# Performance work log

Measured on AMD Instinct MI355X. Metric: run time of the kernel, lower is better.

Reference implementation:

```python
import jax, jax.numpy as jnp
import numpy as np

B, S, H, K = 64, 512, 1024, 7

def setup_inputs() -> dict:
    key = jax.random.key(0)
    ks = jax.random.split(key, 7)
    x = jax.random.normal(ks[0], (B, S, H), dtype=jnp.float32)
    gt = jax.random.randint(ks[1], (B, S), 0, K, dtype=jnp.int64)
    mask = jnp.ones((B, S), dtype=bool)
    # learned parameters
    W = jax.random.normal(ks[2], (H, K), dtype=jnp.float32) * (1.0 / np.sqrt(H))
    b = jnp.zeros((K,), dtype=jnp.float32)
    start_trans = jax.random.uniform(ks[3], (K,), minval=-0.1, maxval=0.1)
    end_trans = jax.random.uniform(ks[4], (K,), minval=-0.1, maxval=0.1)
    trans = jax.random.uniform(ks[5], (K, K), minval=-0.1, maxval=0.1)
    return {"x": x, "gt": gt, "mask": mask, "W": W, "b": b,
            "start_trans": start_trans, "end_trans": end_trans, "trans": trans}

def _crf_neg_llh(emissions, gt, mask, start_trans, end_trans, trans):
    # emissions: [B,S,K], gt: [B,S] int, mask: [B,S] bool
    maskf = mask.astype(emissions.dtype)
    # ---- numerator: score of gold path ----
    em_at_tag = jnp.take_along_axis(emissions, gt[..., None], axis=-1)[..., 0]  # [B,S]
    trans_sc = trans[gt[:, :-1], gt[:, 1:]]                                      # [B,S-1]
    num = start_trans[gt[:, 0]] + em_at_tag[:, 0]
    num = num + jnp.sum((trans_sc + em_at_tag[:, 1:]) * maskf[:, 1:], axis=1)
    last_idx = jnp.sum(mask, axis=1).astype(jnp.int32) - 1                       # [B]
    last_tags = jnp.take_along_axis(gt, last_idx[:, None], axis=1)[:, 0]
    num = num + end_trans[last_tags]
    # ---- denominator: log partition via forward algorithm (lax.scan) ----
    alpha0 = start_trans[None, :] + emissions[:, 0]                              # [B,K]
    em_rest = jnp.transpose(emissions[:, 1:], (1, 0, 2))                         # [S-1,B,K]
    m_rest = jnp.transpose(mask[:, 1:], (1, 0))                                  # [S-1,B]
    def step(alpha, inp):
        em_t, m_t = inp
        nxt = jax.nn.logsumexp(alpha[:, :, None] + trans[None, :, :] + em_t[:, None, :], axis=1)
        return jnp.where(m_t[:, None], nxt, alpha), None
    alpha, _ = jax.lax.scan(step, alpha0, (em_rest, m_rest))
    denom = jax.nn.logsumexp(alpha + end_trans[None, :], axis=1)                 # [B]
    llh = num - denom
    return -jnp.mean(llh)  # reduction='mean', module returns negative

def reference(x, gt, mask, W, b, start_trans, end_trans, trans):
    emissions = jnp.einsum('bsh,hk->bsk', x, W) + b
    return _crf_neg_llh(emissions, gt, mask, start_trans, end_trans, trans)
```

## Files before the change

### kernel.cpp

```cpp
#include <hip/hip_runtime.h>
#include <math.h>

#define NB 64
#define NS 512
#define NH 1024
#define NK 7
#define NCHUNK 16
#define CLEN 32

typedef float f32x4 __attribute__((ext_vector_type(4)));

template <int CTRL>
__device__ __forceinline__ float dpp_add(float v) {
    const int sh = __builtin_amdgcn_update_dpp(0, __float_as_int(v),
                                               CTRL, 0xF, 0xF, true);
    return v + __int_as_float(sh);
}
template <int PAT>
__device__ __forceinline__ float swz_add(float v) {
    const int sh = __builtin_amdgcn_ds_swizzle(__float_as_int(v), PAT);
    return v + __int_as_float(sh);
}

__global__ __launch_bounds__(512) void fused_emis_chunk(
    const float* __restrict__ x, const float* __restrict__ W,
    const float* __restrict__ bias, const float* __restrict__ trans,
    float* __restrict__ em, float* __restrict__ chunkP)
{
    __shared__ float lds_q[CLEN][4][9];
    __shared__ float lds_em[CLEN * 8];
    __shared__ float lds_tr[49];

    const int tid  = threadIdx.x;
    const int lane = tid & 63;
    const int wave = tid >> 6;
    const int q    = wave & 3;
    const int g    = wave >> 2;
    const int b = blockIdx.x >> 4;
    const int c = blockIdx.x & (NCHUNK - 1);
    const int t0 = c * CLEN;
    const int row0 = b * NS + t0;

    if (tid < 49) lds_tr[tid] = trans[tid];

    f32x4 wf0, wf1, wf2, wf3, wf4, wf5, wf6;
    {
        const float* wbase = W + (size_t)28 * (q * 64 + lane);
        asm volatile("global_load_dwordx4 %0, %1, off"            : "=v"(wf0) : "v"(wbase));
        asm volatile("global_load_dwordx4 %0, %1, off offset:16"  : "=v"(wf1) : "v"(wbase));
        asm volatile("global_load_dwordx4 %0, %1, off offset:32"  : "=v"(wf2) : "v"(wbase));
        asm volatile("global_load_dwordx4 %0, %1, off offset:48"  : "=v"(wf3) : "v"(wbase));
        asm volatile("global_load_dwordx4 %0, %1, off offset:64"  : "=v"(wf4) : "v"(wbase));
        asm volatile("global_load_dwordx4 %0, %1, off offset:80"  : "=v"(wf5) : "v"(wbase));
        asm volatile("global_load_dwordx4 %0, %1, off offset:96"  : "=v"(wf6) : "v"(wbase));
        asm volatile("s_waitcnt vmcnt(0)"
                     : "+v"(wf0), "+v"(wf1), "+v"(wf2), "+v"(wf3),
                       "+v"(wf4), "+v"(wf5), "+v"(wf6));
    }
    float wlin[28];
#pragma unroll
    for (int e = 0; e < 4; ++e) {
        wlin[e]      = wf0[e]; wlin[4 + e]  = wf1[e]; wlin[8 + e]  = wf2[e];
        wlin[12 + e] = wf3[e]; wlin[16 + e] = wf4[e]; wlin[20 + e] = wf5[e];
        wlin[24 + e] = wf6[e];
    }
#define WV(i, k) wlin[(i) * 7 + (k)]

    const float4* xq = (const float4*)(x + (size_t)row0 * NH) + q * 64 + lane;
#define PF 4
    float4 xb[PF];
#pragma unroll
    for (int j = 0; j < PF; ++j)
        xb[j] = xq[(size_t)(g + 2 * j) * (NH / 4)];

#pragma unroll
    for (int j = 0; j < 16; ++j) {
        const float4 v = xb[j & (PF - 1)];
        if (j + PF < 16)
            xb[j & (PF - 1)] = xq[(size_t)(g + 2 * (j + PF)) * (NH / 4)];
        float acc[NK];
#pragma unroll
        for (int k = 0; k < NK; ++k)
            acc[k] = v.x * WV(0, k) + v.y * WV(1, k)
                   + v.z * WV(2, k) + v.w * WV(3, k);
#pragma unroll
        for (int k = 0; k < NK; ++k) {
            acc[k] = dpp_add<0xB1>(acc[k]);
            acc[k] = dpp_add<0x4E>(acc[k]);
            acc[k] = dpp_add<0x141>(acc[k]);
        }
        const int ss = lane & 7;
        const float v01 = (ss & 1) ? acc[1] : acc[0];
        const float v23 = (ss & 1) ? acc[3] : acc[2];
        const float v45 = (ss & 1) ? acc[5] : acc[4];
        const float w03 = (ss & 2) ? v23 : v01;
        const float w47 = (ss & 2) ? acc[6] : v45;
        float r8 = (ss & 4) ? w47 : w03;
        r8 = swz_add<0x201F>(r8);
        r8 = swz_add<0x401F>(r8);
        r8 += __shfl_xor(r8, 32, 64);
        if (lane < NK) lds_q[g + 2 * j][q][lane] = r8;
    }
#undef PF
#undef WV
    __syncthreads();

    if (tid < CLEN * NK) {
        const int r = tid / NK;
        const int k = tid - r * NK;
        const float e = lds_q[r][0][k] + lds_q[r][1][k]
                      + lds_q[r][2][k] + lds_q[r][3][k] + bias[k];
        lds_em[r * 8 + k] = e;
        em[(size_t)row0 * NK + tid] = e;
    }
    __syncthreads();
    if (wave != 0) return;

    const int li = lane < 49 ? lane : 48;
    const int i = li / 7;
    const int k = li - i * 7;
    float tj[NK];
#pragma unroll
    for (int j = 0; j < NK; ++j) tj[j] = lds_tr[j * 7 + k];

    const int first = (c == 0) ? 1 : 0;
    float P = lds_tr[i * 7 + k] + lds_em[first * 8 + k];
    for (int t = first + 1; t < CLEN; ++t) {
        float a[NK];
#pragma unroll
        for (int j = 0; j < NK; ++j)
            a[j] = __shfl(P, i * 7 + j, 64) + tj[j];
        const float m = fmaxf(fmaxf(fmaxf(a[0], a[1]), fmaxf(a[2], a[3])),
                              fmaxf(fmaxf(a[4], a[5]), a[6]));
        const float su = __expf(a[0]-m) + __expf(a[1]-m) + __expf(a[2]-m)
                       + __expf(a[3]-m) + __expf(a[4]-m) + __expf(a[5]-m)
                       + __expf(a[6]-m);
        P = m + __logf(su) + lds_em[t * 8 + k];
    }
    if (lane < 49)
        chunkP[(size_t)(b * NCHUNK + c) * 49 + lane] = P;
}

__global__ __launch_bounds__(64) void combine_kernel(
    const float* __restrict__ em, const float* __restrict__ chunkP,
    const int* __restrict__ gt32,
    const float* __restrict__ start_trans, const float* __restrict__ end_trans,
    const float* __restrict__ trans, float* __restrict__ out)
{
    __shared__ float lds_C[NCHUNK * 49];
    __shared__ float lds_tr[49];
    __shared__ int   lds_gt[NS];
    const int b    = blockIdx.x;
    const int lane = threadIdx.x;

    int oddbits = 0;
    for (int i = lane; i < 256; i += 64) oddbits |= gt32[2 * i + 1];
    const bool is64 = (__ballot(oddbits != 0) == 0ull);

    for (int idx = lane; idx < NCHUNK * 49; idx += 64)
        lds_C[idx] = chunkP[(size_t)b * NCHUNK * 49 + idx];
    for (int i = lane; i < NS; i += 64) {
        const int gidx = b * NS + i;
        lds_gt[i] = is64 ? gt32[2 * gidx] : gt32[gidx];
    }
    if (lane < 49) lds_tr[lane] = trans[lane];
    __syncthreads();

    const float* emb = em + (size_t)b * NS * NK;
    float numpart = 0.f;
#pragma unroll
    for (int ii = 0; ii < NS / 64; ++ii) {
        const int t = lane + 64 * ii;
        const int g = lds_gt[t];
        if (t == 0) numpart += start_trans[g] + emb[g];
        else        numpart += lds_tr[lds_gt[t - 1] * 7 + g] + emb[t * NK + g];
    }
#pragma unroll
    for (int m = 1; m < 64; m <<= 1) numpart += __shfl_xor(numpart, m, 64);
    const float num = numpart + end_trans[lds_gt[NS - 1]];

    const int kk = lane < NK ? lane : NK - 1;
    float alpha = start_trans[kk] + emb[kk];
#pragma unroll
    for (int c = 0; c < NCHUNK; ++c) {
        float a[NK];
#pragma unroll
        for (int j = 0; j < NK; ++j)
            a[j] = __shfl(alpha, j, 64) + lds_C[c * 49 + j * 7 + kk];
        const float m = fmaxf(fmaxf(fmaxf(a[0], a[1]), fmaxf(a[2], a[3])),
                              fmaxf(fmaxf(a[4], a[5]), a[6]));
        const float su = __expf(a[0]-m) + __expf(a[1]-m) + __expf(a[2]-m)
                       + __expf(a[3]-m) + __expf(a[4]-m) + __expf(a[5]-m)
                       + __expf(a[6]-m);
        alpha = m + __logf(su);
    }

    float v = (lane < NK) ? (alpha + end_trans[kk]) : -3.0e38f;
    float mv = v;
#pragma unroll
    for (int m = 1; m < 8; m <<= 1) mv = fmaxf(mv, __shfl_xor(mv, m, 64));
    float e = (lane < NK) ? __expf(v - mv) : 0.f;
#pragma unroll
    for (int m = 1; m < 8; m <<= 1) e += __shfl_xor(e, m, 64);
    if (lane == 0)
        atomicAdd(out, ((mv + __logf(e)) - num) * (1.0f / NB));
}

extern "C" void kernel_launch(void* const* d_in, const int* in_sizes, int n_in,
                              void* d_out, int out_size, void* d_ws, size_t ws_size,
                              hipStream_t stream)
{
    const float* x    = (const float*)d_in[0];
    const int*   gt   = (const int*)d_in[1];
    const float* W    = (const float*)d_in[3];
    const float* bias = (const float*)d_in[4];
    const float* st   = (const float*)d_in[5];
    const float* et   = (const float*)d_in[6];
    const float* tr   = (const float*)d_in[7];

    float* em     = (float*)d_ws;
    float* chunkP = em + (size_t)NB * NS * NK;

    (void)hipMemsetAsync(d_out, 0, sizeof(float) * out_size, stream);
    fused_emis_chunk<<<NB * NCHUNK, 512, 0, stream>>>(x, W, bias, tr, em, chunkP);
    combine_kernel<<<NB, 64, 0, stream>>>(em, chunkP, gt, st, et, tr, (float*)d_out);
}
```

Measured before the change: 226.2 us.

## Process two chunks per block and overlap chunk scan with next GEMV

Each block now computes emissions for two consecutive 32-row chunks, halving the grid to 512 blocks. While the other waves compute the second chunk's emissions, wave 0 runs the first chunk's forward scan and gold-path partial score, so the serial scan overlaps with memory-bound work. The per-row emissions are no longer written to global memory. The gold-path numerator is computed per chunk and combined later, which removes the gt and emission reads from the combine kernel. The tradeoffs are half as many blocks to hide latency and a longer serial tail on wave 1 for the second chunk.

```diff
diff --git a/kernel.cpp b/kernel.cpp
--- a/kernel.cpp
+++ b/kernel.cpp
@@ -8,6 +8,10 @@
 #define NCHUNK 16
 #define CLEN 32
 
+#define WS_ALPHA0  0
+#define WS_NUMP    (WS_ALPHA0 + 64 * 8)
+#define WS_CHUNKP  (WS_NUMP + 64 * 16)
+
 typedef float f32x4 __attribute__((ext_vector_type(4)));
 
 template <int CTRL>
@@ -22,62 +26,21 @@
     return v + __int_as_float(sh);
 }
 
-__global__ __launch_bounds__(512) void fused_emis_chunk(
-    const float* __restrict__ x, const float* __restrict__ W,
-    const float* __restrict__ bias, const float* __restrict__ trans,
-    float* __restrict__ em, float* __restrict__ chunkP)
-{
-    __shared__ float lds_q[CLEN][4][9];
-    __shared__ float lds_em[CLEN * 8];
-    __shared__ float lds_tr[49];
-
-    const int tid  = threadIdx.x;
-    const int lane = tid & 63;
-    const int wave = tid >> 6;
-    const int q    = wave & 3;
-    const int g    = wave >> 2;
-    const int b = blockIdx.x >> 4;
-    const int c = blockIdx.x & (NCHUNK - 1);
-    const int t0 = c * CLEN;
-    const int row0 = b * NS + t0;
-
-    if (tid < 49) lds_tr[tid] = trans[tid];
-
-    f32x4 wf0, wf1, wf2, wf3, wf4, wf5, wf6;
-    {
-        const float* wbase = W + (size_t)28 * (q * 64 + lane);
-        asm volatile("global_load_dwordx4 %0, %1, off"            : "=v"(wf0) : "v"(wbase));
-        asm volatile("global_load_dwordx4 %0, %1, off offset:16"  : "=v"(wf1) : "v"(wbase));
-        asm volatile("global_load_dwordx4 %0, %1, off offset:32"  : "=v"(wf2) : "v"(wbase));
-        asm volatile("global_load_dwordx4 %0, %1, off offset:48"  : "=v"(wf3) : "v"(wbase));
-        asm volatile("global_load_dwordx4 %0, %1, off offset:64"  : "=v"(wf4) : "v"(wbase));
-        asm volatile("global_load_dwordx4 %0, %1, off offset:80"  : "=v"(wf5) : "v"(wbase));
-        asm volatile("global_load_dwordx4 %0, %1, off offset:96"  : "=v"(wf6) : "v"(wbase));
-        asm volatile("s_waitcnt vmcnt(0)"
-                     : "+v"(wf0), "+v"(wf1), "+v"(wf2), "+v"(wf3),
-                       "+v"(wf4), "+v"(wf5), "+v"(wf6));
-    }
-    float wlin[28];
-#pragma unroll
-    for (int e = 0; e < 4; ++e) {
-        wlin[e]      = wf0[e]; wlin[4 + e]  = wf1[e]; wlin[8 + e]  = wf2[e];
-        wlin[12 + e] = wf3[e]; wlin[16 + e] = wf4[e]; wlin[20 + e] = wf5[e];
-        wlin[24 + e] = wf6[e];
-    }
+__device__ __forceinline__ void emit_rows(
+    const float* __restrict__ x, size_t row0, int q, int g, int lane,
+    const float (&wlin)[28], float (*lds_q)[4][9])
+{
 #define WV(i, k) wlin[(i) * 7 + (k)]
-
-    const float4* xq = (const float4*)(x + (size_t)row0 * NH) + q * 64 + lane;
-#define PF 4
-    float4 xb[PF];
-#pragma unroll
-    for (int j = 0; j < PF; ++j)
+    const float4* xq = (const float4*)(x + row0 * NH) + q * 64 + lane;
+    float4 xb[4];
+#pragma unroll
+    for (int j = 0; j < 4; ++j)
         xb[j] = xq[(size_t)(g + 2 * j) * (NH / 4)];
-
 #pragma unroll
     for (int j = 0; j < 16; ++j) {
-        const float4 v = xb[j & (PF - 1)];
-        if (j + PF < 16)
-            xb[j & (PF - 1)] = xq[(size_t)(g + 2 * (j + PF)) * (NH / 4)];
+        const float4 v = xb[j & 3];
+        if (j + 4 < 16)
+            xb[j & 3] = xq[(size_t)(g + 2 * (j + 4)) * (NH / 4)];
         float acc[NK];
 #pragma unroll
         for (int k = 0; k < NK; ++k)
@@ -101,30 +64,49 @@
         r8 += __shfl_xor(r8, 32, 64);
         if (lane < NK) lds_q[g + 2 * j][q][lane] = r8;
     }
-#undef PF
 #undef WV
-    __syncthreads();
-
-    if (tid < CLEN * NK) {
-        const int r = tid / NK;
-        const int k = tid - r * NK;
-        const float e = lds_q[r][0][k] + lds_q[r][1][k]
-                      + lds_q[r][2][k] + lds_q[r][3][k] + bias[k];
-        lds_em[r * 8 + k] = e;
-        em[(size_t)row0 * NK + tid] = e;
-    }
-    __syncthreads();
-    if (wave != 0) return;
-
+}
+
+__device__ __forceinline__ void num_partial(
+    const int* __restrict__ gt32, const float* __restrict__ st,
+    const float* __restrict__ et, const float* lds_tr, const float* lem,
+    int b, int ch, int lane, float* __restrict__ numP)
+{
+    int oddbits = 0;
+    for (int i = lane; i < 256; i += 64) oddbits |= gt32[2 * i + 1];
+    const bool is64 = (__ballot(oddbits != 0) == 0ull);
+    const int tloc = lane & 31;
+    const int tg = ch * CLEN + tloc;
+    const int gidx = b * NS + tg;
+    const int g2 = is64 ? gt32[2 * gidx] : gt32[gidx];
+    float term = 0.f;
+    if (lane < 32) {
+        if (tg == 0) {
+            term = st[g2] + lem[g2];
+        } else {
+            const int pidx = gidx - 1;
+            const int gp = is64 ? gt32[2 * pidx] : gt32[pidx];
+            term = lds_tr[gp * 7 + g2] + lem[tloc * 8 + g2];
+        }
+        if (tg == NS - 1) term += et[g2];
+    }
+#pragma unroll
+    for (int m = 1; m < 64; m <<= 1) term += __shfl_xor(term, m, 64);
+    if (lane == 0) numP[b * NCHUNK + ch] = term;
+}
+
+__device__ __forceinline__ void scan_chunk(
+    const float* lds_tr, const float* lem, int b, int ch, int lane,
+    float* __restrict__ chunkP)
+{
     const int li = lane < 49 ? lane : 48;
     const int i = li / 7;
     const int k = li - i * 7;
     float tj[NK];
 #pragma unroll
     for (int j = 0; j < NK; ++j) tj[j] = lds_tr[j * 7 + k];
-
-    const int first = (c == 0) ? 1 : 0;
-    float P = lds_tr[i * 7 + k] + lds_em[first * 8 + k];
+    const int first = (ch == 0) ? 1 : 0;
+    float P = lds_tr[i * 7 + k] + lem[first * 8 + k];
     for (int t = first + 1; t < CLEN; ++t) {
         float a[NK];
 #pragma unroll
@@ -135,52 +117,120 @@
         const float su = __expf(a[0]-m) + __expf(a[1]-m) + __expf(a[2]-m)
                        + __expf(a[3]-m) + __expf(a[4]-m) + __expf(a[5]-m)
                        + __expf(a[6]-m);
-        P = m + __logf(su) + lds_em[t * 8 + k];
+        P = m + __logf(su) + lem[t * 8 + k];
     }
     if (lane < 49)
-        chunkP[(size_t)(b * NCHUNK + c) * 49 + lane] = P;
+        chunkP[(size_t)(b * NCHUNK + ch) * 49 + lane] = P;
+}
+
+__global__ __launch_bounds__(512) void fused_emis_chunk(
+    const float* __restrict__ x, const float* __restrict__ W,
+    const float* __restrict__ bias, const float* __restrict__ trans,
+    const float* __restrict__ start_trans, const float* __restrict__ end_trans,
+    const int* __restrict__ gt32, float* __restrict__ ws)
+{
+    __shared__ float lds_q[CLEN][4][9];
+    __shared__ float lds_em[2][CLEN * 8];
+    __shared__ float lds_tr[49];
+
+    float* __restrict__ alpha0g = ws + WS_ALPHA0;
+    float* __restrict__ numP    = ws + WS_NUMP;
+    float* __restrict__ chunkP  = ws + WS_CHUNKP;
+
+    const int tid  = threadIdx.x;
+    const int lane = tid & 63;
+    const int wave = tid >> 6;
+    const int q    = wave & 3;
+    const int g    = wave >> 2;
+    const int b  = blockIdx.x >> 3;
+    const int cc = blockIdx.x & 7;
+    const int cA = 2 * cc;
+    const int cB = 2 * cc + 1;
+    const size_t row0A = (size_t)b * NS + cA * CLEN;
+    const size_t row0B = (size_t)b * NS + cB * CLEN;
+
+    if (tid < 49) lds_tr[tid] = trans[tid];
+
+    f32x4 wf0, wf1, wf2, wf3, wf4, wf5, wf6;
+    {
+        const float* wbase = W + (size_t)28 * (q * 64 + lane);
+        asm volatile("global_load_dwordx4 %0, %1, off"            : "=v"(wf0) : "v"(wbase));
+        asm volatile("global_load_dwordx4 %0, %1, off offset:16"  : "=v"(wf1) : "v"(wbase));
+        asm volatile("global_load_dwordx4 %0, %1, off offset:32"  : "=v"(wf2) : "v"(wbase));
+        asm volatile("global_load_dwordx4 %0, %1, off offset:48"  : "=v"(wf3) : "v"(wbase));
+        asm volatile("global_load_dwordx4 %0, %1, off offset:64"  : "=v"(wf4) : "v"(wbase));
+        asm volatile("global_load_dwordx4 %0, %1, off offset:80"  : "=v"(wf5) : "v"(wbase));
+        asm volatile("global_load_dwordx4 %0, %1, off offset:96"  : "=v"(wf6) : "v"(wbase));
+        asm volatile("s_waitcnt vmcnt(0)"
+                     : "+v"(wf0), "+v"(wf1), "+v"(wf2), "+v"(wf3),
+                       "+v"(wf4), "+v"(wf5), "+v"(wf6));
+    }
+    float wlin[28];
+#pragma unroll
+    for (int e = 0; e < 4; ++e) {
+        wlin[e]      = wf0[e]; wlin[4 + e]  = wf1[e]; wlin[8 + e]  = wf2[e];
+        wlin[12 + e] = wf3[e]; wlin[16 + e] = wf4[e]; wlin[20 + e] = wf5[e];
+        wlin[24 + e] = wf6[e];
+    }
+
+    emit_rows(x, row0A, q, g, lane, wlin, lds_q);
+    __syncthreads();
+
+    if (tid < CLEN * NK) {
+        const int r = tid / NK;
+        const int k = tid - r * NK;
+        lds_em[0][r * 8 + k] = lds_q[r][0][k] + lds_q[r][1][k]
+                             + lds_q[r][2][k] + lds_q[r][3][k] + bias[k];
+    }
+    __syncthreads();
+
+    if (wave == 0) {
+        if (cc == 0 && lane < NK)
+            alpha0g[b * 8 + lane] = start_trans[lane] + lds_em[0][lane];
+        num_partial(gt32, start_trans, end_trans, lds_tr, lds_em[0],
+                    b, cA, lane, numP);
+        scan_chunk(lds_tr, lds_em[0], b, cA, lane, chunkP);
+    }
+    emit_rows(x, row0B, q, g, lane, wlin, lds_q);
+    __syncthreads();
+
+    if (tid < CLEN * NK) {
+        const int r = tid / NK;
+        const int k = tid - r * NK;
+        lds_em[1][r * 8 + k] = lds_q[r][0][k] + lds_q[r][1][k]
+                             + lds_q[r][2][k] + lds_q[r][3][k] + bias[k];
+    }
+    __syncthreads();
+
+    if (wave == 1) {
+        num_partial(gt32, start_trans, end_trans, lds_tr, lds_em[1],
+                    b, cB, lane, numP);
+        scan_chunk(lds_tr, lds_em[1], b, cB, lane, chunkP);
+    }
 }
 
 __global__ __launch_bounds__(64) void combine_kernel(
-    const float* __restrict__ em, const float* __restrict__ chunkP,
-    const int* __restrict__ gt32,
-    const float* __restrict__ start_trans, const float* __restrict__ end_trans,
-    const float* __restrict__ trans, float* __restrict__ out)
+    const float* __restrict__ ws, const float* __restrict__ end_trans,
+    float* __restrict__ out)
 {
     __shared__ float lds_C[NCHUNK * 49];
-    __shared__ float lds_tr[49];
-    __shared__ int   lds_gt[NS];
+    const float* __restrict__ alpha0g = ws + WS_ALPHA0;
+    const float* __restrict__ numP    = ws + WS_NUMP;
+    const float* __restrict__ chunkP  = ws + WS_CHUNKP;
     const int b    = blockIdx.x;
     const int lane = threadIdx.x;
 
-    int oddbits = 0;
-    for (int i = lane; i < 256; i += 64) oddbits |= gt32[2 * i + 1];
-    const bool is64 = (__ballot(oddbits != 0) == 0ull);
-
     for (int idx = lane; idx < NCHUNK * 49; idx += 64)
         lds_C[idx] = chunkP[(size_t)b * NCHUNK * 49 + idx];
-    for (int i = lane; i < NS; i += 64) {
-        const int gidx = b * NS + i;
-        lds_gt[i] = is64 ? gt32[2 * gidx] : gt32[gidx];
-    }
-    if (lane < 49) lds_tr[lane] = trans[lane];
-    __syncthreads();
-
-    const float* emb = em + (size_t)b * NS * NK;
-    float numpart = 0.f;
-#pragma unroll
-    for (int ii = 0; ii < NS / 64; ++ii) {
-        const int t = lane + 64 * ii;
-        const int g = lds_gt[t];
-        if (t == 0) numpart += start_trans[g] + emb[g];
-        else        numpart += lds_tr[lds_gt[t - 1] * 7 + g] + emb[t * NK + g];
-    }
-#pragma unroll
-    for (int m = 1; m < 64; m <<= 1) numpart += __shfl_xor(numpart, m, 64);
-    const float num = numpart + end_trans[lds_gt[NS - 1]];
+    __syncthreads();
+
+    float np = (lane < NCHUNK) ? numP[b * NCHUNK + lane] : 0.f;
+#pragma unroll
+    for (int m = 1; m < 16; m <<= 1) np += __shfl_xor(np, m, 64);
+    const float num = __shfl(np, 0, 64);
 
     const int kk = lane < NK ? lane : NK - 1;
-    float alpha = start_trans[kk] + emb[kk];
+    float alpha = alpha0g[b * 8 + kk];
 #pragma unroll
     for (int c = 0; c < NCHUNK; ++c) {
         float a[NK];
@@ -218,10 +268,10 @@
     const float* et   = (const float*)d_in[6];
     const float* tr   = (const float*)d_in[7];
 
-    float* em     = (float*)d_ws;
-    float* chunkP = em + (size_t)NB * NS * NK;
+    float* ws = (float*)d_ws;
 
     (void)hipMemsetAsync(d_out, 0, sizeof(float) * out_size, stream);
-    fused_emis_chunk<<<NB * NCHUNK, 512, 0, stream>>>(x, W, bias, tr, em, chunkP);
-    combine_kernel<<<NB, 64, 0, stream>>>(em, chunkP, gt, st, et, tr, (float*)d_out);
-}
+    fused_emis_chunk<<<NB * (NCHUNK / 2), 512, 0, stream>>>(
+        x, W, bias, tr, st, et, gt, ws);
+    combine_kernel<<<NB, 64, 0, stream>>>(ws, et, (float*)d_out);
+}
```

New measurement: 228.1 us. Within noise of the previous version (+0.9%).
